# Optimization experiments

Hardware: AMD Instinct MI355X
Metric: run time of the kernel (lower is better)

Reference implementation:

```python
import jax, jax.numpy as jnp
import numpy as np

B, S, D = 2, 2048, 2048
H, DK, DV = 16, 128, 128
K_DIM = H * DK
V_DIM = H * DV
CONV_DIM = 2 * K_DIM + V_DIM
KS = 4
EPS = 1e-6


def setup_inputs() -> dict:
    key = jax.random.key(0)
    ks = jax.random.split(key, 9)
    sc = lambda k, shape, s=0.02: jax.random.normal(k, shape, jnp.float32) * s
    return {
        "hidden_states": jax.random.normal(ks[0], (B, S, D), jnp.float32),
        "attention_mask": jnp.ones((B, S), jnp.float32),
        "W_qkv": sc(ks[1], (CONV_DIM, D)),
        "conv_w": sc(ks[2], (CONV_DIM, 1, KS), 0.2),   # depthwise kernel [C,1,K]
        "conv_b": jnp.zeros((CONV_DIM,), jnp.float32),
        "W_z": sc(ks[3], (V_DIM, D)),
        "W_b": sc(ks[4], (H, D)),
        "W_a": sc(ks[5], (H, D)),
        "dt_bias": jnp.ones((H,), jnp.float32),
        "A_log": jnp.log(jax.random.uniform(ks[6], (H,), jnp.float32, 0.5, 8.0)),
        "norm_weight": jnp.zeros((DV,), jnp.float32),
        "W_out": sc(ks[7], (D, V_DIM)),
    }


def _l2norm(x):
    return x * jax.lax.rsqrt(jnp.sum(x * x, -1, keepdims=True) + 1e-6)


def _gated_delta_rule(q, k, v, g, beta):
    # q,k: [B,S,H,DK]; v: [B,S,H,DV]; g,beta: [B,S,H]
    q = _l2norm(q) * (DK ** -0.5)
    k = _l2norm(k)

    def step(state, inp):
        # state: [B,H,DK,DV]
        qt, kt, vt, gt, bt = inp
        state = state * jnp.exp(gt)[..., None, None]          # gated decay
        kv = jnp.einsum('bhk,bhkv->bhv', kt, state)           # k^T S
        delta = (vt - kv) * bt[..., None]                     # delta-rule correction
        state = state + kt[..., :, None] * delta[..., None, :]
        ot = jnp.einsum('bhk,bhkv->bhv', qt, state)
        return state, ot

    xs = tuple(jnp.moveaxis(a, 1, 0) for a in (q, k, v, g, beta))  # time-major
    state0 = jnp.zeros((B, H, DK, DV), jnp.float32)
    _, o = jax.lax.scan(step, state0, xs)
    return jnp.moveaxis(o, 0, 1)  # [B,S,H,DV]


def reference(hidden_states, attention_mask, W_qkv, conv_w, conv_b, W_z, W_b,
              W_a, dt_bias, A_log, norm_weight, W_out):
    x = hidden_states * attention_mask[:, :, None]
    mixed = jnp.einsum('bsd,cd->bsc', x, W_qkv)               # [B,S,CONV_DIM]
    # causal depthwise conv over time
    xc = jnp.moveaxis(mixed, 1, 2)                            # [B,C,S]
    xc = jax.lax.conv_general_dilated(xc, conv_w, (1,), [(KS - 1, 0)],
                                      feature_group_count=CONV_DIM)
    xc = xc + conv_b[None, :, None]
    mixed = jax.nn.silu(jnp.moveaxis(xc, 2, 1))               # [B,S,C]
    q, k, v = jnp.split(mixed, [K_DIM, 2 * K_DIM], axis=-1)
    q = q.reshape(B, S, H, DK)
    k = k.reshape(B, S, H, DK)
    v = v.reshape(B, S, H, DV)
    z = jnp.einsum('bsd,vd->bsv', x, W_z).reshape(B, S, H, DV)
    beta = jax.nn.sigmoid(jnp.einsum('bsd,hd->bsh', x, W_b))
    g = -jnp.exp(A_log) * jax.nn.softplus(jnp.einsum('bsd,hd->bsh', x, W_a) + dt_bias)
    o = _gated_delta_rule(q, k, v, g, beta)                   # [B,S,H,DV]
    # gated RMSNorm over head_v_dim
    o = o * jax.lax.rsqrt(jnp.mean(o * o, -1, keepdims=True) + EPS)
    o = o * (1.0 + norm_weight)
    o = o * jax.nn.silu(z)
    return jnp.einsum('bsv,dv->bsd', o.reshape(B, S, V_DIM), W_out)
```

## Files before the change

### kernel.cpp

```cpp
#include <hip/hip_runtime.h>
#include <hip/hip_bf16.h>
#include <math.h>

#define BB 2
#define SS 2048
#define DD 2048
#define HH 16
#define CONVC 6144
#define MM (BB*SS)

#define CH 64
#define NCH 32
#define CD_KTS 0
#define CD_TV  16384
#define CD_TP  32768
#define CD_AQ  40960
#define CD_PV  49152
#define CD_PC  49408
#define CD_STRIDE 49664

typedef __bf16 bf16_t;
typedef __bf16 bf16x8 __attribute__((ext_vector_type(8)));
typedef __bf16 bf16x4 __attribute__((ext_vector_type(4)));
typedef float  f32x4  __attribute__((ext_vector_type(4)));

#define GLOBAL_AS __attribute__((address_space(1)))
#define LDS_AS    __attribute__((address_space(3)))

#define MFMA16(a,b,c) __builtin_amdgcn_mfma_f32_16x16x32_bf16((a),(b),(c),0,0,0)

__global__ __launch_bounds__(256) void cast_all_kernel(
    const float* __restrict__ hs, const float* __restrict__ amask,
    const float* __restrict__ Wqkv, const float* __restrict__ Wz,
    const float* __restrict__ Wb, const float* __restrict__ Wa,
    const float* __restrict__ Wout,
    bf16_t* __restrict__ x_bf, bf16_t* __restrict__ wB,
    bf16_t* __restrict__ wba, bf16_t* __restrict__ woutb)
{
  const long N0 = (long)MM*DD/4;
  const long N1 = N0 + (long)CONVC*DD/4;
  const long N2 = N1 + (long)DD*DD/4;
  const long N3 = N2 + 16*DD/4;
  const long N4 = N3 + 16*DD/4;
  const long N5 = N4 + (long)DD*DD/4;
  for (long i = (long)blockIdx.x*256 + threadIdx.x; i < N5; i += (long)gridDim.x*256) {
    const float* src; bf16_t* dst; float m = 1.f;
    if (i < N0)      { long j=i;    src = hs   + j*4; dst = x_bf + j*4; m = amask[(j*4)/DD]; }
    else if (i < N1) { long j=i-N0; src = Wqkv + j*4; dst = wB + j*4; }
    else if (i < N2) { long j=i-N1; src = Wz   + j*4; dst = wB + (size_t)CONVC*DD + j*4; }
    else if (i < N3) { long j=i-N2; src = Wb   + j*4; dst = wba + j*4; }
    else if (i < N4) { long j=i-N3; src = Wa   + j*4; dst = wba + 16*DD + j*4; }
    else             { long j=i-N4; src = Wout + j*4; dst = woutb + j*4; }
    float4 v = *(const float4*)src;
    bf16x4 o4;
    o4[0]=(bf16_t)(v.x*m); o4[1]=(bf16_t)(v.y*m);
    o4[2]=(bf16_t)(v.z*m); o4[3]=(bf16_t)(v.w*m);
    *(bf16x4*)dst = o4;
  }
}

__global__ __launch_bounds__(64) void betag3_kernel(
    const bf16_t* __restrict__ xbf, const bf16_t* __restrict__ wba,
    const float* __restrict__ dtb, const float* __restrict__ Alog,
    float2* __restrict__ gb_t)
{
  const int blk = blockIdx.x;
  const int lane = threadIdx.x;
  const int fr = lane & 15, fq = lane >> 4;
  const long tok0 = (long)blk*16;

  f32x4 acc0 = {0,0,0,0}, acc1 = {0,0,0,0};
  const bf16_t* ar = xbf + (tok0 + fr)*DD + fq*8;
  const bf16_t* b0 = wba + fr*DD + fq*8;
  const bf16_t* b1 = wba + (16+fr)*DD + fq*8;
  #pragma unroll 4
  for (int ks=0; ks<64; ++ks) {
    bf16x8 a8 = *(const bf16x8*)(ar + ks*32);
    bf16x8 p8 = *(const bf16x8*)(b0 + ks*32);
    bf16x8 q8 = *(const bf16x8*)(b1 + ks*32);
    acc0 = MFMA16(a8, p8, acc0);
    acc1 = MFMA16(a8, q8, acc1);
  }
  const int h = fr;
  float eA = expf(Alog[h]);
  float db = dtb[h];
  #pragma unroll
  for (int r=0;r<4;r++) {
    long tok = tok0 + fq*4 + r;
    int b = (int)(tok >> 11), s = (int)(tok & (SS-1));
    float beta = 1.f/(1.f+expf(-acc0[r]));
    float tt2 = acc1[r] + db;
    float sp = (tt2 > 20.f) ? tt2 : log1pf(expf(tt2));
    float g  = -eA * sp;
    gb_t[((long)b*HH + h)*SS + s] = make_float2(g, beta);
  }
}

__global__ __launch_bounds__(512) void gemm_fused(
    const bf16_t* __restrict__ A, const bf16_t* __restrict__ Bm,
    bf16_t* __restrict__ Cmix, bf16_t* __restrict__ Cz, int K, int nbn)
{
  extern __shared__ char gsm[];
  const int t    = threadIdx.x;
  const int lane = t & 63;
  const int wid  = t >> 6;
  const int wm   = wid >> 2, wn = wid & 3;
  const int fr   = lane & 15, fq = lane >> 4;

  const int nwg = gridDim.x;
  const int wg  = ((int)blockIdx.x & 7)*(nwg >> 3) + ((int)blockIdx.x >> 3);
  const int grp = wg / (nbn*4);
  const int rem = wg - grp*(nbn*4);
  const long bm = grp*4 + (rem & 3);
  const long bn = rem >> 2;

  int rowS[2], colS[2];
  #pragma unroll
  for (int i=0;i<2;i++) {
    int L  = (i*512 + t)*16;
    int Ls = L ^ (((L>>9)&1)<<5);
    rowS[i] = (Ls>>10)*16 + ((Ls&1023)>>6);
    colS[i] = (Ls&63)>>1;
  }
  const bf16_t* Ab = A  + (bm*256)*(long)K;
  const bf16_t* Bb = Bm + (bn*256)*(long)K;

  f32x4 acc[8][4];
  #pragma unroll
  for (int i=0;i<8;i++)
    #pragma unroll
    for (int j=0;j<4;j++) acc[i][j] = (f32x4){0.f,0.f,0.f,0.f};

  const int aoff = fr*64 + ((fq*16) ^ ((fr&8)<<2));

  auto stage = [&](int buf, int oper, int kh, int kt) {
    const bf16_t* srcb = oper ? Bb : Ab;
    char* dst0 = gsm + oper*65536 + buf*32768 + kh*16384 + t*16;
    #pragma unroll
    for (int i=0;i<2;i++) {
      const bf16_t* src = srcb + (long)rowS[i]*K + kt*64 + kh*32 + colS[i];
      __builtin_amdgcn_global_load_lds((const GLOBAL_AS void*)src,
          (LDS_AS void*)(dst0 + i*8192), 16, 0, 0);
    }
  };

  stage(0,0,0,0); stage(0,1,0,0); stage(0,0,1,0); stage(0,1,1,0);
  asm volatile("s_waitcnt vmcnt(4)" ::: "memory");
  __builtin_amdgcn_s_barrier();

  bf16x8 bfr[4];
  int cb = 0;
  const int KT = K >> 6;
  for (int kt=0; kt<KT; ++kt) {
    const int ktn = (kt+1 < KT) ? kt+1 : kt;
    const char* abuf = gsm + cb*32768;
    const char* bbuf = gsm + 65536 + cb*32768;

    #pragma unroll
    for (int ph=0; ph<4; ph++) {
      const int kh = ph >> 1, mh = ph & 1;
      bf16x8 af[4];
      #pragma unroll
      for (int j=0;j<4;j++)
        af[j] = *(const bf16x8*)(abuf + kh*16384 + (wm*8 + mh*4 + j)*1024 + aoff);
      if (mh == 0) {
        #pragma unroll
        for (int n=0;n<4;n++)
          bfr[n] = *(const bf16x8*)(bbuf + kh*16384 + (wn*4+n)*1024 + aoff);
      }
      stage(cb^1, mh, kh, ktn);
      if (mh == 1) {
        __builtin_amdgcn_sched_barrier(0);
        asm volatile("s_waitcnt vmcnt(4)" ::: "memory");
      }
      __builtin_amdgcn_sched_barrier(0);
      __builtin_amdgcn_s_barrier();
      asm volatile("s_waitcnt lgkmcnt(0)" ::: "memory");
      __builtin_amdgcn_sched_barrier(0);
      __builtin_amdgcn_s_setprio(1);
      #pragma unroll
      for (int j=0;j<4;j++)
        #pragma unroll
        for (int n=0;n<4;n++)
          acc[mh*4+j][n] = MFMA16(af[j], bfr[n], acc[mh*4+j][n]);
      __builtin_amdgcn_s_setprio(0);
    }
    cb ^= 1;
  }
  __syncthreads();

  bf16_t* Co;
  long No, colb;
  if (bn < 24) { Co = Cmix; No = CONVC; colb = bn*256; }
  else         { Co = Cz;   No = DD;    colb = (bn-24)*256; }

  #pragma unroll
  for (int mi=0;mi<8;mi++) {
    #pragma unroll
    for (int ni=0;ni<4;ni++) {
      long row = bm*256 + wm*128 + mi*16 + fq*4;
      long col = colb + wn*64 + ni*16 + fr;
      #pragma unroll
      for (int r=0;r<4;r++)
        Co[(row+r)*No + col] = (bf16_t)acc[mi][ni][r];
    }
  }
}

template<bool OUT_BF16>
__global__ __launch_bounds__(512) void gemm256(
    const bf16_t* __restrict__ A, const bf16_t* __restrict__ Bm,
    void* __restrict__ Cp, int M, int N, int K, int nbn)
{
  extern __shared__ char gsm[];
  const int t    = threadIdx.x;
  const int lane = t & 63;
  const int wid  = t >> 6;
  const int wm   = wid >> 2, wn = wid & 3;
  const int fr   = lane & 15, fq = lane >> 4;

  const int nwg = gridDim.x;
  const int wg  = ((int)blockIdx.x & 7)*(nwg >> 3) + ((int)blockIdx.x >> 3);
  const int grp = wg / (nbn*4);
  const int rem = wg - grp*(nbn*4);
  const long bm = grp*4 + (rem & 3);
  const long bn = rem >> 2;

  int rowS[2], colS[2];
  #pragma unroll
  for (int i=0;i<2;i++) {
    int L  = (i*512 + t)*16;
    int Ls = L ^ (((L>>9)&1)<<5);
    rowS[i] = (Ls>>10)*16 + ((Ls&1023)>>6);
    colS[i] = (Ls&63)>>1;
  }
  const bf16_t* Ab = A  + (bm*256)*(long)K;
  const bf16_t* Bb = Bm + (bn*128)*(long)K;

  f32x4 acc[8][2];
  #pragma unroll
  for (int i=0;i<8;i++) { acc[i][0] = (f32x4){0,0,0,0}; acc[i][1] = (f32x4){0,0,0,0}; }

  const int aoff = fr*64 + ((fq*16) ^ ((fr&8)<<2));

  auto stageA = [&](int buf, int kh, int kt) {
    char* dst0 = gsm + buf*32768 + kh*16384 + t*16;
    #pragma unroll
    for (int i=0;i<2;i++) {
      const bf16_t* src = Ab + (long)rowS[i]*K + kt*64 + kh*32 + colS[i];
      __builtin_amdgcn_global_load_lds((const GLOBAL_AS void*)src,
          (LDS_AS void*)(dst0 + i*8192), 16, 0, 0);
    }
  };
  auto stageB = [&](int buf, int kh, int kt) {
    char* dst = gsm + 65536 + buf*16384 + kh*8192 + t*16;
    const bf16_t* src = Bb + (long)rowS[0]*K + kt*64 + kh*32 + colS[0];
    __builtin_amdgcn_global_load_lds((const GLOBAL_AS void*)src,
        (LDS_AS void*)dst, 16, 0, 0);
  };

  stageA(0,0,0); stageB(0,0,0); stageA(0,1,0); stageB(0,1,0);
  asm volatile("s_waitcnt vmcnt(3)" ::: "memory");
  __builtin_amdgcn_s_barrier();

  int cb = 0;
  const int KT = K >> 6;
  for (int kt=0; kt<KT; ++kt) {
    const int ktn = (kt+1 < KT) ? kt+1 : kt;
    const char* abuf = gsm + cb*32768;
    const char* bbuf = gsm + 65536 + cb*16384;

    #pragma unroll
    for (int kh=0; kh<2; kh++) {
      bf16x8 af[8], bfr[2];
      #pragma unroll
      for (int j=0;j<8;j++)
        af[j] = *(const bf16x8*)(abuf + kh*16384 + (wm*8+j)*1024 + aoff);
      #pragma unroll
      for (int n=0;n<2;n++)
        bfr[n] = *(const bf16x8*)(bbuf + kh*8192 + (wn*2+n)*1024 + aoff);
      stageA(cb^1, kh, ktn);
      stageB(cb^1, kh, ktn);
      asm volatile("s_waitcnt vmcnt(3)" ::: "memory");
      __builtin_amdgcn_sched_barrier(0);
      __builtin_amdgcn_s_barrier();
      asm volatile("s_waitcnt lgkmcnt(0)" ::: "memory");
      __builtin_amdgcn_sched_barrier(0);
      __builtin_amdgcn_s_setprio(1);
      #pragma unroll
      for (int j=0;j<8;j++)
        #pragma unroll
        for (int n=0;n<2;n++)
          acc[j][n] = MFMA16(af[j], bfr[n], acc[j][n]);
      __builtin_amdgcn_s_setprio(0);
    }
    cb ^= 1;
  }
  __syncthreads();

  #pragma unroll
  for (int mi=0;mi<8;mi++) {
    #pragma unroll
    for (int ni=0;ni<2;ni++) {
      long row = bm*256 + wm*128 + mi*16 + fq*4;
      long col = bn*128 + wn*32 + ni*16 + fr;
      #pragma unroll
      for (int r=0;r<4;r++) {
        float v = acc[mi][ni][r];
        if (OUT_BF16) ((bf16_t*)Cp)[(row+r)*(long)N + col] = (bf16_t)v;
        else          ((float*)Cp)[(row+r)*(long)N + col] = v;
      }
    }
  }
}

__global__ __launch_bounds__(256) void conv_norm_kernel(
    const bf16_t* __restrict__ mixed, const float* __restrict__ cw,
    const float* __restrict__ cb, bf16_t* __restrict__ q_t,
    bf16_t* __restrict__ k_t, bf16_t* __restrict__ v_t)
{
  __shared__ bf16_t lx[35*392];
  __shared__ float4 lcw[384];
  __shared__ float  lcb[384];
  const int blk = blockIdx.x;
  const int st = blk & 63;
  const int h  = (blk >> 6) & 15;
  const int b  = blk >> 10;
  const int t  = threadIdx.x;
  const int s0 = st*32;

  for (int i = t; i < 384; i += 256) {
    int seg = i >> 7, d = i & 127;
    int gch = seg*2048 + h*128 + d;
    lcw[i] = ((const float4*)cw)[gch];
    lcb[i] = cb[gch];
  }
  for (int idx = t; idx < 1680; idx += 256) {
    int chunk = idx >> 4, e = idx & 15;
    int row = chunk / 3, seg = chunk - row*3;
    int s2 = s0 - 3 + row;
    bf16x8 v8;
    if (s2 >= 0) {
      v8 = *(const bf16x8*)(mixed + ((long)b*SS + s2)*CONVC + seg*2048 + h*128 + e*8);
    } else {
      #pragma unroll
      for (int j=0;j<8;j++) v8[j] = (bf16_t)0.f;
    }
    *(bf16x8*)&lx[row*392 + seg*128 + e*8] = v8;
  }
  __syncthreads();

  const int s_local = t >> 3, dg = t & 7;
  const int s  = s0 + s_local;
  const int d0 = dg*16;
  const long obase = ((long)(b*HH + h)*SS + s)*128 + d0;

  float scl_q = 0.f, scl_k = 0.f;

  #pragma unroll
  for (int seg=0; seg<3; ++seg) {
    bf16x8 xr[4][2];
    #pragma unroll
    for (int tp=0; tp<4; ++tp) {
      const bf16_t* p = &lx[(s_local + tp)*392 + seg*128 + d0];
      xr[tp][0] = *(const bf16x8*)p;
      xr[tp][1] = *(const bf16x8*)(p + 8);
    }
    float a[16];
    #pragma unroll
    for (int half=0; half<2; ++half) {
      #pragma unroll
      for (int j=0;j<8;j++) {
        int ch = seg*128 + d0 + half*8 + j;
        float4 wj = lcw[ch];
        float v = lcb[ch]
                + (float)xr[0][half][j]*wj.x + (float)xr[1][half][j]*wj.y
                + (float)xr[2][half][j]*wj.z + (float)xr[3][half][j]*wj.w;
        a[half*8+j] = v * (1.f/(1.f+expf(-v)));
      }
    }
    if (seg < 2) {
      float ss = 0.f;
      #pragma unroll
      for (int j=0;j<16;j++) ss += a[j]*a[j];
      ss += __shfl_xor(ss, 1);
      ss += __shfl_xor(ss, 2);
      ss += __shfl_xor(ss, 4);
      float scl = rsqrtf(ss + 1e-6f);
      if (seg == 0) scl_q = scl * 0.08838834764831845f;
      else          scl_k = scl;
    }
    {
      bf16_t* outp = (seg==0) ? (q_t + obase) : (seg==1) ? (k_t + obase) : (v_t + obase);
      float scl = (seg==0) ? scl_q : (seg==1) ? scl_k : 1.f;
      bf16x8 o0, o1;
      #pragma unroll
      for (int j=0;j<8;j++) { o0[j] = (bf16_t)(a[j]*scl); o1[j] = (bf16_t)(a[8+j]*scl); }
      *(bf16x8*)outp = o0;
      *(bf16x8*)(outp + 8) = o1;
    }
  }
}

__global__ __launch_bounds__(256) void chunkA_kernel(
    const bf16_t* __restrict__ q_t, const bf16_t* __restrict__ k_t,
    const bf16_t* __restrict__ v_t, const float2* __restrict__ gb_t,
    char* __restrict__ cdata)
{
  extern __shared__ char smem[];
  bf16_t* lK  = (bf16_t*)(smem);
  bf16_t* lQV = (bf16_t*)(smem + 17408);
  float*  lLf = (float*)(smem + 35840);
  float*  lXf = (float*)(smem + 52480);
  float*  gcv = (float*)(smem + 69120);
  float*  pvv = (float*)(smem + 69376);
  float*  bvv = (float*)(smem + 69632);
  float*  evv = (float*)(smem + 69888);
  float*  lP  = (float*)(smem + 70144);

  const int cd = blockIdx.x;
  const int bh = cd >> 5, c = cd & 31;
  const int t = threadIdx.x;
  const int lane = t & 63, w = t >> 6;
  const int fr = lane & 15, fq = lane >> 4;

  const bf16_t* kg = k_t + ((long)bh*SS + c*CH)*128;
  const bf16_t* qg = q_t + ((long)bh*SS + c*CH)*128;
  const bf16_t* vg = v_t + ((long)bh*SS + c*CH)*128;
  char* cdp = cdata + (long)cd*CD_STRIDE;

  #pragma unroll
  for (int ib=0; ib<4; ib++) {
    int e0 = (t + 256*ib)*8;
    int r = e0 >> 7, cc = e0 & 127;
    *(bf16x8*)&lK[r*136+cc]  = *(const bf16x8*)(kg + e0);
    *(bf16x8*)&lQV[r*136+cc] = *(const bf16x8*)(qg + e0);
  }
  if (t < 64) {
    float2 gb = gb_t[(long)bh*SS + c*CH + t];
    gcv[t] = gb.x;
    bvv[t] = gb.y;
  }
  __syncthreads();
  if (t < 64) {
    float g = gcv[t];
    #pragma unroll
    for (int off=1; off<64; off<<=1) {
      float n = __shfl_up(g, off);
      if (lane >= off) g += n;
    }
    gcv[t] = g;
  }
  __syncthreads();
  if (t < 64) {
    pvv[t] = expf(gcv[t]);
    evv[t] = expf(gcv[63] - gcv[t]);
  }

  {
    f32x4 accG[4], accQ[4];
    #pragma unroll
    for (int tn=0;tn<4;tn++){ accG[tn]=(f32x4){0,0,0,0}; accQ[tn]=(f32x4){0,0,0,0}; }
    #pragma unroll
    for (int ks=0;ks<4;ks++) {
      bf16x8 aK = *(const bf16x8*)&lK[(w*16+fr)*136 + fq*8 + ks*32];
      bf16x8 aQ = *(const bf16x8*)&lQV[(w*16+fr)*136 + fq*8 + ks*32];
      #pragma unroll
      for (int tn=0;tn<4;tn++) {
        bf16x8 bK = *(const bf16x8*)&lK[(tn*16+fr)*136 + fq*8 + ks*32];
        accG[tn] = MFMA16(aK, bK, accG[tn]);
        accQ[tn] = MFMA16(aQ, bK, accQ[tn]);
      }
    }
    bf16_t* aqg = (bf16_t*)(cdp + CD_AQ);
    #pragma unroll
    for (int tn=0;tn<4;tn++) {
      #pragma unroll
      for (int r=0;r<4;r++) {
        int tt = w*16 + fq*4 + r;
        int ii = tn*16 + fr;
        float er = expf(gcv[tt] - gcv[ii]);
        lLf[tt*65 + ii] = (ii < tt) ? bvv[tt]*er*accG[tn][r] : 0.f;
        aqg[tt*64 + ii] = (bf16_t)((ii <= tt) ? er*accQ[tn][r] : 0.f);
      }
    }
  }

  {
    const int a = w;
    float* Ub = lXf + (a*16)*65 + a*16;
    const float* Lb = lLf + (a*16)*65 + a*16;
    if (lane < 16) Ub[lane] = (lane == 0) ? 1.f : 0.f;
    for (int bb = a+1; bb < 4; bb++)
      for (int e = lane; e < 256; e += 64)
        lXf[(a*16 + (e>>4))*65 + bb*16 + (e&15)] = 0.f;
    if (lane < 16) {
      const int cc = lane;
      for (int i=1; i<16; i++) {
        float s = 0.f;
        for (int j=0; j<i; j++) s += Lb[i*65+j] * Ub[j*65+cc];
        Ub[i*65+cc] = ((i==cc)?1.f:0.f) - s;
      }
    }
  }
  __syncthreads();

  bf16_t* lVT = lQV;
  {
    const int m = t & 15;
    #pragma unroll
    for (int ib=0; ib<4; ib++) {
      int e0 = (t + 256*ib)*8;
      int r = e0 >> 7, cc = e0 & 127;
      bf16x8 v8 = *(const bf16x8*)(vg + e0);
      #pragma unroll
      for (int e=0;e<8;e++) {
        int ee = (e + m) & 7;
        lVT[(cc+ee)*72 + r] = v8[ee];
      }
    }
  }

  {
    const int i = t >> 4, j = t & 15;
    #pragma unroll
    for (int bb=0; bb<3; bb++) {
      float s = 0.f;
      const float* Mrow = lLf + ((bb+1)*16 + i)*65 + bb*16;
      const float* Ucol = lXf + (bb*16)*65 + bb*16 + j;
      #pragma unroll
      for (int k=0;k<16;k++) s += Mrow[k] * Ucol[k*65];
      lP[bb*272 + i*17 + j] = s;
    }
  }
  __syncthreads();
  {
    const int i = t >> 4, j = t & 15;
    #pragma unroll
    for (int bb=0; bb<3; bb++) {
      float s = 0.f;
      const float* Urow = lXf + ((bb+1)*16 + i)*65 + (bb+1)*16;
      const float* Pcol = lP + bb*272 + j;
      #pragma unroll
      for (int k=0;k<16;k++) s += Urow[k] * Pcol[k*17];
      lXf[((bb+1)*16 + i)*65 + bb*16 + j] = -s;
    }
  }
  __syncthreads();
  {
    const int i = t >> 4, j = t & 15;
    #pragma unroll
    for (int bb=0; bb<2; bb++) {
      float s = 0.f;
      const float* M0 = lLf + ((bb+2)*16 + i)*65 + bb*16;
      const float* U0 = lXf + (bb*16)*65 + bb*16 + j;
      const float* M1 = lLf + ((bb+2)*16 + i)*65 + (bb+1)*16;
      const float* T1 = lXf + ((bb+1)*16)*65 + bb*16 + j;
      #pragma unroll
      for (int k=0;k<16;k++) s += M0[k]*U0[k*65] + M1[k]*T1[k*65];
      lP[bb*272 + i*17 + j] = s;
    }
  }
  __syncthreads();
  {
    const int i = t >> 4, j = t & 15;
    #pragma unroll
    for (int bb=0; bb<2; bb++) {
      float s = 0.f;
      const float* Urow = lXf + ((bb+2)*16 + i)*65 + (bb+2)*16;
      const float* Pcol = lP + bb*272 + j;
      #pragma unroll
      for (int k=0;k<16;k++) s += Urow[k] * Pcol[k*17];
      lXf[((bb+2)*16 + i)*65 + bb*16 + j] = -s;
    }
  }
  __syncthreads();
  {
    const int i = t >> 4, j = t & 15;
    float s = 0.f;
    const float* M0 = lLf + (48 + i)*65 + 0;
    const float* U0 = lXf + 0*65 + j;
    const float* M1 = lLf + (48 + i)*65 + 16;
    const float* T1 = lXf + 16*65 + j;
    const float* M2 = lLf + (48 + i)*65 + 32;
    const float* T2 = lXf + 32*65 + j;
    #pragma unroll
    for (int k=0;k<16;k++) s += M0[k]*U0[k*65] + M1[k]*T1[k*65] + M2[k]*T2[k*65];
    lP[i*17 + j] = s;
  }
  __syncthreads();
  {
    const int i = t >> 4, j = t & 15;
    float s = 0.f;
    const float* Urow = lXf + (48 + i)*65 + 48;
    const float* Pcol = lP + j;
    #pragma unroll
    for (int k=0;k<16;k++) s += Urow[k] * Pcol[k*17];
    lXf[(48 + i)*65 + j] = -s;
  }
  __syncthreads();

  bf16_t* lXb = (bf16_t*)lLf;
  {
    bf16_t* tpg = (bf16_t*)(cdp + CD_TP);
    #pragma unroll
    for (int ib=0; ib<16; ib++) {
      int idx = t + ib*256; int r = idx>>6, cc = idx&63;
      float xv = lXf[r*65+cc] * bvv[cc];
      tpg[r*64+cc] = (bf16_t)(xv * pvv[cc]);
      lXb[r*72+cc] = (bf16_t)xv;
    }
  }
  __syncthreads();

  {
    f32x4 acc[8];
    #pragma unroll
    for (int tn=0;tn<8;tn++) acc[tn]=(f32x4){0,0,0,0};
    #pragma unroll
    for (int ks=0;ks<2;ks++) {
      bf16x8 aX = *(const bf16x8*)&lXb[(w*16+fr)*72 + fq*8 + ks*32];
      #pragma unroll
      for (int tn=0;tn<8;tn++) {
        bf16x8 bV = *(const bf16x8*)&lVT[(tn*16+fr)*72 + fq*8 + ks*32];
        acc[tn] = MFMA16(aX, bV, acc[tn]);
      }
    }
    bf16_t* tvg = (bf16_t*)(cdp + CD_TV);
    #pragma unroll
    for (int tn=0;tn<8;tn++)
      #pragma unroll
      for (int r=0;r<4;r++) {
        int tt = w*16 + fq*4 + r, dv = tn*16 + fr;
        tvg[tt*128 + dv] = (bf16_t)acc[tn][r];
      }
  }

  {
    bf16_t* ktg = (bf16_t*)(cdp + CD_KTS);
    int dk = t >> 1, c0 = (t & 1)*32;
    bf16_t tmp[32];
    #pragma unroll
    for (int i2=0;i2<32;i2++) {
      int i = c0 + i2;
      tmp[i2] = (bf16_t)((float)lK[i*136 + dk] * evv[i]);
    }
    #pragma unroll
    for (int s8=0;s8<4;s8++)
      *(bf16x8*)&ktg[dk*64 + c0 + s8*8] = *(bf16x8*)&tmp[s8*8];
  }
  if (t < 64) ((float*)(cdp + CD_PV))[t] = pvv[t];
  if (t == 0) *((float*)(cdp + CD_PC)) = expf(gcv[63]);
}

__global__ __launch_bounds__(256) void chunkS_kernel(
    const bf16_t* __restrict__ q_t, const bf16_t* __restrict__ k_t,
    const char* __restrict__ cdata, bf16_t* __restrict__ obuf)
{
  extern __shared__ char smem[];
  float*  lS  = (float*)(smem);
  bf16_t* lSb = (bf16_t*)(smem + 8320);
  bf16_t* lK  = (bf16_t*)(smem + 12672);
  bf16_t* lQ  = (bf16_t*)(smem + 30080);
  bf16_t* lTp = (bf16_t*)(smem + 47488);
  bf16_t* lKT = (bf16_t*)(smem + 56704);
  bf16_t* lXT = (bf16_t*)(smem + 75136);
  bf16_t* lDT = (bf16_t*)(smem + 77952);
  bf16_t* lAq = (bf16_t*)(smem + 80768);

  const int bid = blockIdx.x;
  const int lb  = (bid & 7)*32 + (bid >> 3);
  const int bh = lb >> 3, sp = lb & 7;
  const int dv0 = sp*16;
  const int b = bh >> 4, h = bh & 15;
  const int t = threadIdx.x, lane = t & 63, w = t >> 6;
  const int fr = lane & 15, fq = lane >> 4;

  #pragma unroll
  for (int ib=0; ib<8; ib++) {
    int idx = t + ib*256; int r = idx>>7, cc = idx&127;
    lS[r*129+cc] = 0.f;
    lSb[r*136+cc] = (bf16_t)0.f;
  }

  const bf16_t* kg = k_t + (long)bh*SS*128;
  const bf16_t* qg = q_t + (long)bh*SS*128;

  bf16x8 kr0,kr1,kr2,kr3, qr0,qr1,qr2,qr3, kt0,kt1,kt2,kt3, tp0,tp1, aq0,aq1;

#define STAGE_LOAD(CSRC)                                                       \
  {                                                                            \
    const char* cdl = cdata + (long)(bh*NCH + (CSRC))*CD_STRIDE;               \
    const bf16_t* kl = kg + (long)(CSRC)*CH*128;                               \
    const bf16_t* ql = qg + (long)(CSRC)*CH*128;                               \
    const bf16_t* ktl = (const bf16_t*)(cdl + CD_KTS);                         \
    const bf16_t* tpl = (const bf16_t*)(cdl + CD_TP);                          \
    const bf16_t* aql = (const bf16_t*)(cdl + CD_AQ);                          \
    int e0 = t*8, e1 = (t+256)*8, e2 = (t+512)*8, e3 = (t+768)*8;              \
    kr0 = *(const bf16x8*)(kl + e0); kr1 = *(const bf16x8*)(kl + e1);          \
    kr2 = *(const bf16x8*)(kl + e2); kr3 = *(const bf16x8*)(kl + e3);          \
    qr0 = *(const bf16x8*)(ql + e0); qr1 = *(const bf16x8*)(ql + e1);          \
    qr2 = *(const bf16x8*)(ql + e2); qr3 = *(const bf16x8*)(ql + e3);          \
    kt0 = *(const bf16x8*)(ktl + e0); kt1 = *(const bf16x8*)(ktl + e1);        \
    kt2 = *(const bf16x8*)(ktl + e2); kt3 = *(const bf16x8*)(ktl + e3);        \
    tp0 = *(const bf16x8*)(tpl + e0); tp1 = *(const bf16x8*)(tpl + e1);        \
    aq0 = *(const bf16x8*)(aql + e0); aq1 = *(const bf16x8*)(aql + e1);        \
  }

#define STAGE_WRITE()                                                          \
  {                                                                            \
    int e0 = t*8, e1 = (t+256)*8, e2 = (t+512)*8, e3 = (t+768)*8;              \
    *(bf16x8*)&lK[(e0>>7)*136 + (e0&127)] = kr0;                               \
    *(bf16x8*)&lK[(e1>>7)*136 + (e1&127)] = kr1;                               \
    *(bf16x8*)&lK[(e2>>7)*136 + (e2&127)] = kr2;                               \
    *(bf16x8*)&lK[(e3>>7)*136 + (e3&127)] = kr3;                               \
    *(bf16x8*)&lQ[(e0>>7)*136 + (e0&127)] = qr0;                               \
    *(bf16x8*)&lQ[(e1>>7)*136 + (e1&127)] = qr1;                               \
    *(bf16x8*)&lQ[(e2>>7)*136 + (e2&127)] = qr2;                               \
    *(bf16x8*)&lQ[(e3>>7)*136 + (e3&127)] = qr3;                               \
    *(bf16x8*)&lKT[(e0>>6)*72 + (e0&63)] = kt0;                                \
    *(bf16x8*)&lKT[(e1>>6)*72 + (e1&63)] = kt1;                                \
    *(bf16x8*)&lKT[(e2>>6)*72 + (e2&63)] = kt2;                                \
    *(bf16x8*)&lKT[(e3>>6)*72 + (e3&63)] = kt3;                                \
    *(bf16x8*)&lTp[(e0>>6)*72 + (e0&63)] = tp0;                                \
    *(bf16x8*)&lTp[(e1>>6)*72 + (e1&63)] = tp1;                                \
    *(bf16x8*)&lAq[(e0>>6)*72 + (e0&63)] = aq0;                                \
    *(bf16x8*)&lAq[(e1>>6)*72 + (e1&63)] = aq1;                                \
  }

  STAGE_LOAD(0);
  STAGE_WRITE();
  __syncthreads();

  for (int c=0; c<NCH; c++) {
    const int cd = bh*NCH + c;
    const char* cdp = cdata + (long)cd*CD_STRIDE;

    float tvq0, tvq1, tvq2, tvq3, pc;
    float pvq[4];
    {
      const bf16_t* tvp = (const bf16_t*)(cdp + CD_TV);
      const float* pvp = (const float*)(cdp + CD_PV);
      tvq0 = (float)tvp[(w*16+fq*4+0)*128 + dv0 + fr];
      tvq1 = (float)tvp[(w*16+fq*4+1)*128 + dv0 + fr];
      tvq2 = (float)tvp[(w*16+fq*4+2)*128 + dv0 + fr];
      tvq3 = (float)tvp[(w*16+fq*4+3)*128 + dv0 + fr];
      #pragma unroll
      for (int r=0;r<4;r++) pvq[r] = pvp[w*16+fq*4+r];
      pc = *(const float*)(cdp + CD_PC);
    }
    const int cn = (c+1 < NCH) ? c+1 : c;
    STAGE_LOAD(cn);

    f32x4 aX = {0,0,0,0}, aXq = {0,0,0,0};
    #pragma unroll
    for (int ks=0; ks<4; ks++) {
      bf16x8 bS = *(const bf16x8*)&lSb[fr*136 + fq*8 + ks*32];
      bf16x8 aK = *(const bf16x8*)&lK[(w*16+fr)*136 + fq*8 + ks*32];
      bf16x8 aQ = *(const bf16x8*)&lQ[(w*16+fr)*136 + fq*8 + ks*32];
      aX  = MFMA16(aK, bS, aX);
      aXq = MFMA16(aQ, bS, aXq);
    }
    #pragma unroll
    for (int r=0;r<4;r++)
      lXT[fr*88 + (w*16+fq*4+r)] = (bf16_t)aX[r];
    __syncthreads();

    {
      f32x4 aD = {0,0,0,0};
      #pragma unroll
      for (int ks=0; ks<2; ks++) {
        bf16x8 aT = *(const bf16x8*)&lTp[(w*16+fr)*72 + fq*8 + ks*32];
        bf16x8 bX = *(const bf16x8*)&lXT[fr*88 + fq*8 + ks*32];
        aD = MFMA16(aT, bX, aD);
      }
      lDT[fr*88 + (w*16+fq*4+0)] = (bf16_t)(tvq0 - aD[0]);
      lDT[fr*88 + (w*16+fq*4+1)] = (bf16_t)(tvq1 - aD[1]);
      lDT[fr*88 + (w*16+fq*4+2)] = (bf16_t)(tvq2 - aD[2]);
      lDT[fr*88 + (w*16+fq*4+3)] = (bf16_t)(tvq3 - aD[3]);
    }
    #pragma unroll
    for (int ib=0; ib<8; ib++) {
      int idx = t + ib*256; int r = idx>>7, cc = idx&127;
      lS[r*129+cc] *= pc;
    }
    __syncthreads();

    {
      f32x4 aS0 = {0,0,0,0}, aS1 = {0,0,0,0}, aO = {0,0,0,0};
      #pragma unroll
      for (int ks=0; ks<2; ks++) {
        bf16x8 aDd = *(const bf16x8*)&lDT[fr*88 + fq*8 + ks*32];
        bf16x8 bK0 = *(const bf16x8*)&lKT[(w*32+fr)*72 + fq*8 + ks*32];
        bf16x8 bK1 = *(const bf16x8*)&lKT[(w*32+16+fr)*72 + fq*8 + ks*32];
        bf16x8 aA  = *(const bf16x8*)&lAq[(w*16+fr)*72 + fq*8 + ks*32];
        bf16x8 bD  = *(const bf16x8*)&lDT[fr*88 + fq*8 + ks*32];
        aS0 = MFMA16(aDd, bK0, aS0);
        aS1 = MFMA16(aDd, bK1, aS1);
        aO  = MFMA16(aA,  bD,  aO);
      }
      #pragma unroll
      for (int r=0;r<4;r++) {
        lS[(fq*4+r)*129 + w*32 + fr]      += aS0[r];
        lS[(fq*4+r)*129 + w*32 + 16 + fr] += aS1[r];
      }
      #pragma unroll
      for (int r=0;r<4;r++) {
        int tt = w*16+fq*4+r;
        long tok = (long)b*SS + c*CH + tt;
        float ov = pvq[r]*aXq[r] + aO[r];
        obuf[(tok*HH + h)*128 + dv0 + fr] = (bf16_t)ov;
      }
    }
    __syncthreads();

    STAGE_WRITE();
    #pragma unroll
    for (int ib=0; ib<8; ib++) {
      int idx = t + ib*256; int r = idx>>7, cc = idx&127;
      lSb[r*136+cc] = (bf16_t)lS[r*129+cc];
    }
    __syncthreads();
  }
#undef STAGE_LOAD
#undef STAGE_WRITE
}

__global__ __launch_bounds__(128) void norm_gate_kernel(
    const bf16_t* __restrict__ o, const bf16_t* __restrict__ zfull,
    const float* __restrict__ nw, bf16_t* __restrict__ og)
{
  const long row = blockIdx.x;
  const long tok = row >> 4;
  const int h = row & 15;
  const int d = threadIdx.x;
  float x = (float)o[row*128 + d];
  float ss = x*x;
  #pragma unroll
  for (int off=32; off>=1; off>>=1) ss += __shfl_xor(ss, off);
  __shared__ float red[2];
  if ((d & 63) == 0) red[d>>6] = ss;
  __syncthreads();
  float mean = (red[0] + red[1]) * (1.f/128.f);
  float zn = (float)zfull[tok*DD + h*128 + d];
  float val = x * rsqrtf(mean + 1e-6f) * (1.f + nw[d]) * (zn * (1.f/(1.f+expf(-zn))));
  og[row*128 + d] = (bf16_t)val;
}

extern "C" void kernel_launch(void* const* d_in, const int* in_sizes, int n_in,
                              void* d_out, int out_size, void* d_ws, size_t ws_size,
                              hipStream_t stream)
{
  const float* hs    = (const float*)d_in[0];
  const float* amask = (const float*)d_in[1];
  const float* Wqkv  = (const float*)d_in[2];
  const float* convw = (const float*)d_in[3];
  const float* convb = (const float*)d_in[4];
  const float* Wz    = (const float*)d_in[5];
  const float* Wb    = (const float*)d_in[6];
  const float* Wa    = (const float*)d_in[7];
  const float* dtb   = (const float*)d_in[8];
  const float* Alog  = (const float*)d_in[9];
  const float* nw    = (const float*)d_in[10];
  const float* Wout  = (const float*)d_in[11];

  const size_t MB = 1024*1024;
  char* p = (char*)d_ws;
  auto alloc = [&](size_t bytes) { char* r = p; p += (bytes + 255) & ~(size_t)255; return r; };
  bf16_t* x_bf   = (bf16_t*)alloc(16*MB);
  char*   bigreg = alloc(84*MB);
  bf16_t* wba    = (bf16_t*)alloc(256*1024);
  bf16_t* woutb  = (bf16_t*)alloc(8*MB);
  bf16_t* zbuf   = (bf16_t*)alloc(16*MB);
  bf16_t* q_t    = (bf16_t*)alloc(16*MB);
  bf16_t* k_t    = (bf16_t*)alloc(16*MB);
  bf16_t* v_t    = (bf16_t*)alloc(16*MB);
  float2* gb_t   = (float2*)alloc((size_t)BB*HH*SS*8);
  size_t need = (size_t)(p - (char*)d_ws);
  if (ws_size < need) return;

  bf16_t* wB      = (bf16_t*)bigreg;
  bf16_t* mixed   = (bf16_t*)(bigreg + 34*MB);
  char*   cdata   = bigreg;
  bf16_t* obuf    = v_t;
  bf16_t* og      = q_t;

  cast_all_kernel<<<2048, 256, 0, stream>>>(hs, amask, Wqkv, Wz, Wb, Wa, Wout,
                                            x_bf, wB, wba, woutb);

  betag3_kernel<<<MM/16, 64, 0, stream>>>(x_bf, wba, dtb, Alog, gb_t);

  gemm_fused<<<512, 512, 131072, stream>>>(x_bf, wB, mixed, zbuf, DD, 32);

  conv_norm_kernel<<<BB*HH*(SS/32), 256, 0, stream>>>(mixed, convw, convb, q_t, k_t, v_t);

  chunkA_kernel<<<BB*HH*NCH, 256, 73408, stream>>>(q_t, k_t, v_t, gb_t, cdata);
  chunkS_kernel<<<BB*HH*8, 256, 89984, stream>>>(q_t, k_t, cdata, obuf);

  norm_gate_kernel<<<MM*HH, 128, 0, stream>>>(obuf, zbuf, nw, og);

  gemm256<false><<<256, 512, 98304, stream>>>(og, woutb, d_out, MM, DD, DD, 16);
}
```

Before: 381.5 us.

## Double-buffer chunk state-scan LDS stages and vectorize norm-gate kernel

```diff
diff --git a/kernel.cpp b/kernel.cpp
--- a/kernel.cpp
+++ b/kernel.cpp
@@ -22,6 +22,7 @@
 typedef __bf16 bf16_t;
 typedef __bf16 bf16x8 __attribute__((ext_vector_type(8)));
 typedef __bf16 bf16x4 __attribute__((ext_vector_type(4)));
+typedef __bf16 bf16x2 __attribute__((ext_vector_type(2)));
 typedef float  f32x4  __attribute__((ext_vector_type(4)));
 
 #define GLOBAL_AS __attribute__((address_space(1)))
@@ -660,13 +661,8 @@
   extern __shared__ char smem[];
   float*  lS  = (float*)(smem);
   bf16_t* lSb = (bf16_t*)(smem + 8320);
-  bf16_t* lK  = (bf16_t*)(smem + 12672);
-  bf16_t* lQ  = (bf16_t*)(smem + 30080);
-  bf16_t* lTp = (bf16_t*)(smem + 47488);
-  bf16_t* lKT = (bf16_t*)(smem + 56704);
-  bf16_t* lXT = (bf16_t*)(smem + 75136);
-  bf16_t* lDT = (bf16_t*)(smem + 77952);
-  bf16_t* lAq = (bf16_t*)(smem + 80768);
+  bf16_t* lXT = (bf16_t*)(smem + 137600);
+  bf16_t* lDT = (bf16_t*)(smem + 140416);
 
   const int bid = blockIdx.x;
   const int lb  = (bid & 7)*32 + (bid >> 3);
@@ -686,7 +682,7 @@
   const bf16_t* kg = k_t + (long)bh*SS*128;
   const bf16_t* qg = q_t + (long)bh*SS*128;
 
-  bf16x8 kr0,kr1,kr2,kr3, qr0,qr1,qr2,qr3, kt0,kt1,kt2,kt3, tp0,tp1, aq0,aq1;
+  bf16x8 kr0,kr1,kr2,kr3, qr0,qr1,qr2,qr3, kt0,kt1,kt2,kt3, tp0,tp1;
 
 #define STAGE_LOAD(CSRC)                                                       \
   {                                                                            \
@@ -695,7 +691,6 @@
     const bf16_t* ql = qg + (long)(CSRC)*CH*128;                               \
     const bf16_t* ktl = (const bf16_t*)(cdl + CD_KTS);                         \
     const bf16_t* tpl = (const bf16_t*)(cdl + CD_TP);                          \
-    const bf16_t* aql = (const bf16_t*)(cdl + CD_AQ);                          \
     int e0 = t*8, e1 = (t+256)*8, e2 = (t+512)*8, e3 = (t+768)*8;              \
     kr0 = *(const bf16x8*)(kl + e0); kr1 = *(const bf16x8*)(kl + e1);          \
     kr2 = *(const bf16x8*)(kl + e2); kr3 = *(const bf16x8*)(kl + e3);          \
@@ -704,43 +699,53 @@
     kt0 = *(const bf16x8*)(ktl + e0); kt1 = *(const bf16x8*)(ktl + e1);        \
     kt2 = *(const bf16x8*)(ktl + e2); kt3 = *(const bf16x8*)(ktl + e3);        \
     tp0 = *(const bf16x8*)(tpl + e0); tp1 = *(const bf16x8*)(tpl + e1);        \
-    aq0 = *(const bf16x8*)(aql + e0); aq1 = *(const bf16x8*)(aql + e1);        \
-  }
-
-#define STAGE_WRITE()                                                          \
+  }
+
+#define STAGE_WRITE(BASE)                                                      \
   {                                                                            \
+    char* _bp = (BASE);                                                        \
+    bf16_t* _lK  = (bf16_t*)_bp;                                               \
+    bf16_t* _lQ  = (bf16_t*)(_bp + 17408);                                     \
+    bf16_t* _lTp = (bf16_t*)(_bp + 34816);                                     \
+    bf16_t* _lKT = (bf16_t*)(_bp + 44032);                                     \
     int e0 = t*8, e1 = (t+256)*8, e2 = (t+512)*8, e3 = (t+768)*8;              \
-    *(bf16x8*)&lK[(e0>>7)*136 + (e0&127)] = kr0;                               \
-    *(bf16x8*)&lK[(e1>>7)*136 + (e1&127)] = kr1;                               \
-    *(bf16x8*)&lK[(e2>>7)*136 + (e2&127)] = kr2;                               \
-    *(bf16x8*)&lK[(e3>>7)*136 + (e3&127)] = kr3;                               \
-    *(bf16x8*)&lQ[(e0>>7)*136 + (e0&127)] = qr0;                               \
-    *(bf16x8*)&lQ[(e1>>7)*136 + (e1&127)] = qr1;                               \
-    *(bf16x8*)&lQ[(e2>>7)*136 + (e2&127)] = qr2;                               \
-    *(bf16x8*)&lQ[(e3>>7)*136 + (e3&127)] = qr3;                               \
-    *(bf16x8*)&lKT[(e0>>6)*72 + (e0&63)] = kt0;                                \
-    *(bf16x8*)&lKT[(e1>>6)*72 + (e1&63)] = kt1;                                \
-    *(bf16x8*)&lKT[(e2>>6)*72 + (e2&63)] = kt2;                                \
-    *(bf16x8*)&lKT[(e3>>6)*72 + (e3&63)] = kt3;                                \
-    *(bf16x8*)&lTp[(e0>>6)*72 + (e0&63)] = tp0;                                \
-    *(bf16x8*)&lTp[(e1>>6)*72 + (e1&63)] = tp1;                                \
-    *(bf16x8*)&lAq[(e0>>6)*72 + (e0&63)] = aq0;                                \
-    *(bf16x8*)&lAq[(e1>>6)*72 + (e1&63)] = aq1;                                \
+    *(bf16x8*)&_lK[(e0>>7)*136 + (e0&127)] = kr0;                              \
+    *(bf16x8*)&_lK[(e1>>7)*136 + (e1&127)] = kr1;                              \
+    *(bf16x8*)&_lK[(e2>>7)*136 + (e2&127)] = kr2;                              \
+    *(bf16x8*)&_lK[(e3>>7)*136 + (e3&127)] = kr3;                              \
+    *(bf16x8*)&_lQ[(e0>>7)*136 + (e0&127)] = qr0;                              \
+    *(bf16x8*)&_lQ[(e1>>7)*136 + (e1&127)] = qr1;                              \
+    *(bf16x8*)&_lQ[(e2>>7)*136 + (e2&127)] = qr2;                              \
+    *(bf16x8*)&_lQ[(e3>>7)*136 + (e3&127)] = qr3;                              \
+    *(bf16x8*)&_lKT[(e0>>6)*72 + (e0&63)] = kt0;                               \
+    *(bf16x8*)&_lKT[(e1>>6)*72 + (e1&63)] = kt1;                               \
+    *(bf16x8*)&_lKT[(e2>>6)*72 + (e2&63)] = kt2;                               \
+    *(bf16x8*)&_lKT[(e3>>6)*72 + (e3&63)] = kt3;                               \
+    *(bf16x8*)&_lTp[(e0>>6)*72 + (e0&63)] = tp0;                               \
+    *(bf16x8*)&_lTp[(e1>>6)*72 + (e1&63)] = tp1;                               \
   }
 
   STAGE_LOAD(0);
-  STAGE_WRITE();
+  STAGE_WRITE(smem + 12672);
   __syncthreads();
 
   for (int c=0; c<NCH; c++) {
     const int cd = bh*NCH + c;
     const char* cdp = cdata + (long)cd*CD_STRIDE;
+    const int cb = c & 1;
+    char* rbuf = smem + 12672 + cb*62464;
+    bf16_t* lK  = (bf16_t*)rbuf;
+    bf16_t* lQ  = (bf16_t*)(rbuf + 17408);
+    bf16_t* lTp = (bf16_t*)(rbuf + 34816);
+    bf16_t* lKT = (bf16_t*)(rbuf + 44032);
 
     float tvq0, tvq1, tvq2, tvq3, pc;
     float pvq[4];
+    bf16x8 aqr0, aqr1;
     {
       const bf16_t* tvp = (const bf16_t*)(cdp + CD_TV);
       const float* pvp = (const float*)(cdp + CD_PV);
+      const bf16_t* aqp = (const bf16_t*)(cdp + CD_AQ);
       tvq0 = (float)tvp[(w*16+fq*4+0)*128 + dv0 + fr];
       tvq1 = (float)tvp[(w*16+fq*4+1)*128 + dv0 + fr];
       tvq2 = (float)tvp[(w*16+fq*4+2)*128 + dv0 + fr];
@@ -748,6 +753,8 @@
       #pragma unroll
       for (int r=0;r<4;r++) pvq[r] = pvp[w*16+fq*4+r];
       pc = *(const float*)(cdp + CD_PC);
+      aqr0 = *(const bf16x8*)(aqp + (w*16+fr)*64 + fq*8);
+      aqr1 = *(const bf16x8*)(aqp + (w*16+fr)*64 + fq*8 + 32);
     }
     const int cn = (c+1 < NCH) ? c+1 : c;
     STAGE_LOAD(cn);
@@ -779,12 +786,9 @@
       lDT[fr*88 + (w*16+fq*4+2)] = (bf16_t)(tvq2 - aD[2]);
       lDT[fr*88 + (w*16+fq*4+3)] = (bf16_t)(tvq3 - aD[3]);
     }
-    #pragma unroll
-    for (int ib=0; ib<8; ib++) {
-      int idx = t + ib*256; int r = idx>>7, cc = idx&127;
-      lS[r*129+cc] *= pc;
-    }
     __syncthreads();
+
+    STAGE_WRITE(smem + 12672 + (cb^1)*62464);
 
     {
       f32x4 aS0 = {0,0,0,0}, aS1 = {0,0,0,0}, aO = {0,0,0,0};
@@ -793,7 +797,7 @@
         bf16x8 aDd = *(const bf16x8*)&lDT[fr*88 + fq*8 + ks*32];
         bf16x8 bK0 = *(const bf16x8*)&lKT[(w*32+fr)*72 + fq*8 + ks*32];
         bf16x8 bK1 = *(const bf16x8*)&lKT[(w*32+16+fr)*72 + fq*8 + ks*32];
-        bf16x8 aA  = *(const bf16x8*)&lAq[(w*16+fr)*72 + fq*8 + ks*32];
+        bf16x8 aA  = (ks==0) ? aqr0 : aqr1;
         bf16x8 bD  = *(const bf16x8*)&lDT[fr*88 + fq*8 + ks*32];
         aS0 = MFMA16(aDd, bK0, aS0);
         aS1 = MFMA16(aDd, bK1, aS1);
@@ -801,8 +805,13 @@
       }
       #pragma unroll
       for (int r=0;r<4;r++) {
-        lS[(fq*4+r)*129 + w*32 + fr]      += aS0[r];
-        lS[(fq*4+r)*129 + w*32 + 16 + fr] += aS1[r];
+        int dvr = fq*4 + r;
+        float s0 = lS[dvr*129 + w*32 + fr]      * pc + aS0[r];
+        float s1 = lS[dvr*129 + w*32 + 16 + fr] * pc + aS1[r];
+        lS[dvr*129 + w*32 + fr]      = s0;
+        lS[dvr*129 + w*32 + 16 + fr] = s1;
+        lSb[dvr*136 + w*32 + fr]      = (bf16_t)s0;
+        lSb[dvr*136 + w*32 + 16 + fr] = (bf16_t)s1;
       }
       #pragma unroll
       for (int r=0;r<4;r++) {
@@ -813,38 +822,31 @@
       }
     }
     __syncthreads();
-
-    STAGE_WRITE();
-    #pragma unroll
-    for (int ib=0; ib<8; ib++) {
-      int idx = t + ib*256; int r = idx>>7, cc = idx&127;
-      lSb[r*136+cc] = (bf16_t)lS[r*129+cc];
-    }
-    __syncthreads();
   }
 #undef STAGE_LOAD
 #undef STAGE_WRITE
 }
 
-__global__ __launch_bounds__(128) void norm_gate_kernel(
+__global__ __launch_bounds__(256) void norm_gate_kernel(
     const bf16_t* __restrict__ o, const bf16_t* __restrict__ zfull,
     const float* __restrict__ nw, bf16_t* __restrict__ og)
 {
-  const long row = blockIdx.x;
+  const long row = (long)blockIdx.x*4 + (threadIdx.x >> 6);
+  const int lane = threadIdx.x & 63;
   const long tok = row >> 4;
   const int h = row & 15;
-  const int d = threadIdx.x;
-  float x = (float)o[row*128 + d];
-  float ss = x*x;
+  bf16x2 xv = *(const bf16x2*)(o + row*128 + lane*2);
+  float x0 = (float)xv[0], x1 = (float)xv[1];
+  float ss = x0*x0 + x1*x1;
   #pragma unroll
   for (int off=32; off>=1; off>>=1) ss += __shfl_xor(ss, off);
-  __shared__ float red[2];
-  if ((d & 63) == 0) red[d>>6] = ss;
-  __syncthreads();
-  float mean = (red[0] + red[1]) * (1.f/128.f);
-  float zn = (float)zfull[tok*DD + h*128 + d];
-  float val = x * rsqrtf(mean + 1e-6f) * (1.f + nw[d]) * (zn * (1.f/(1.f+expf(-zn))));
-  og[row*128 + d] = (bf16_t)val;
+  float rr = rsqrtf(ss*(1.f/128.f) + 1e-6f);
+  bf16x2 zv = *(const bf16x2*)(zfull + tok*DD + h*128 + lane*2);
+  float z0 = (float)zv[0], z1 = (float)zv[1];
+  float v0 = x0 * rr * (1.f + nw[lane*2])   * (z0 * (1.f/(1.f+expf(-z0))));
+  float v1 = x1 * rr * (1.f + nw[lane*2+1]) * (z1 * (1.f/(1.f+expf(-z1))));
+  bf16x2 ov; ov[0] = (bf16_t)v0; ov[1] = (bf16_t)v1;
+  *(bf16x2*)(og + row*128 + lane*2) = ov;
 }
 
 extern "C" void kernel_launch(void* const* d_in, const int* in_sizes, int n_in,
@@ -895,9 +897,9 @@
   conv_norm_kernel<<<BB*HH*(SS/32), 256, 0, stream>>>(mixed, convw, convb, q_t, k_t, v_t);
 
   chunkA_kernel<<<BB*HH*NCH, 256, 73408, stream>>>(q_t, k_t, v_t, gb_t, cdata);
-  chunkS_kernel<<<BB*HH*8, 256, 89984, stream>>>(q_t, k_t, cdata, obuf);
-
-  norm_gate_kernel<<<MM*HH, 128, 0, stream>>>(obuf, zbuf, nw, og);
+  chunkS_kernel<<<BB*HH*8, 256, 143232, stream>>>(q_t, k_t, cdata, obuf);
+
+  norm_gate_kernel<<<MM*HH/4, 256, 0, stream>>>(obuf, zbuf, nw, og);
 
   gemm256<false><<<256, 512, 98304, stream>>>(og, woutb, d_out, MM, DD, DD, 16);
 }
```

Result: faster. 366.9 us (-3.8%).
